# Performance work log

Measured on AMD Instinct MI355X. Metric: run time of the kernel, lower is better.

## Reference

```python
import jax, jax.numpy as jnp
import numpy as np

RNN_DIMS = 1024
FC_DIMS = 1024
N_CLASSES = 256
BATCH = 128


def setup_inputs() -> dict:
    key = jax.random.key(0)
    ks = jax.random.split(key, 10)
    s = 1.0 / np.sqrt(RNN_DIMS)
    inp = {
        "x": jax.random.normal(ks[0], (BATCH, RNN_DIMS), dtype=jnp.float32),
        "h1": jax.random.normal(ks[1], (BATCH, RNN_DIMS), dtype=jnp.float32),
        # GRUCell params (PyTorch layout: [3*H, H] stacked as r,z,n)
        "w_ih": jax.random.uniform(ks[2], (3 * RNN_DIMS, RNN_DIMS), jnp.float32, -s, s),
        "w_hh": jax.random.uniform(ks[3], (3 * RNN_DIMS, RNN_DIMS), jnp.float32, -s, s),
        "b_ih": jax.random.uniform(ks[4], (3 * RNN_DIMS,), jnp.float32, -s, s),
        "b_hh": jax.random.uniform(ks[5], (3 * RNN_DIMS,), jnp.float32, -s, s),
        "w_fc1": jax.random.uniform(ks[6], (FC_DIMS, RNN_DIMS), jnp.float32, -s, s),
        "b_fc1": jax.random.uniform(ks[7], (FC_DIMS,), jnp.float32, -s, s),
        "w_fc3": jax.random.uniform(ks[8], (N_CLASSES, FC_DIMS), jnp.float32, -1.0 / np.sqrt(FC_DIMS), 1.0 / np.sqrt(FC_DIMS)),
        "b_fc3": jax.random.uniform(ks[9], (N_CLASSES,), jnp.float32, -1.0 / np.sqrt(FC_DIMS), 1.0 / np.sqrt(FC_DIMS)),
    }
    return inp


def reference(x, h1, w_ih, w_hh, b_ih, b_hh, w_fc1, b_fc1, w_fc3, b_fc3):
    # --- GRUCell (PyTorch semantics) ---
    gi = x @ w_ih.T + b_ih          # [B, 3H]
    gh = h1 @ w_hh.T + b_hh         # [B, 3H]
    i_r, i_z, i_n = jnp.split(gi, 3, axis=-1)
    h_r, h_z, h_n = jnp.split(gh, 3, axis=-1)
    r = jax.nn.sigmoid(i_r + h_r)
    z = jax.nn.sigmoid(i_z + h_z)
    n = jnp.tanh(i_n + r * h_n)
    h1_prime = (1.0 - z) * n + z * h1   # [B, H]
    # --- residual + MLP head ---
    res = h1_prime + x
    relu1 = jax.nn.relu(res @ w_fc1.T + b_fc1)   # [B, FC]
    out = relu1 @ w_fc3.T + b_fc3                # [B, N_CLASSES]
    return (out, h1_prime)
```

## Files before the change

kernel.cpp:

```cpp
#include <hip/hip_runtime.h>
#include <math.h>

typedef short bf16x8 __attribute__((ext_vector_type(8)));
typedef float f32x4 __attribute__((ext_vector_type(4)));

__device__ __forceinline__ int cvt2(float lo, float hi) {
    int r;
    asm("v_cvt_pk_bf16_f32 %0, %1, %2" : "=v"(r) : "v"(lo), "v"(hi));
    return r;
}

#define BAR() do {                                                        \
        asm volatile("s_waitcnt lgkmcnt(0)" ::: "memory");                \
        __builtin_amdgcn_s_barrier();                                     \
        __builtin_amdgcn_sched_barrier(0);                                \
    } while (0)

__global__ __launch_bounds__(256, 2) void gates_k(
    const float* __restrict__ x, const float* __restrict__ h1,
    const float* __restrict__ w_ih, const float* __restrict__ w_hh,
    const float* __restrict__ b_ih, const float* __restrict__ b_hh,
    float* __restrict__ h1p, float* __restrict__ res,
    float* __restrict__ zf1p, float* __restrict__ zout)
{
    __shared__ short As[2][128 * 64];
    __shared__ short Ws[2][96 * 64];
    const int tid  = threadIdx.x;
    const int lane = tid & 63;
    const int wv   = tid >> 6;

    {
        int id = blockIdx.x * 256 + tid;
        f32x4 z = {};
        *(f32x4*)(zf1p + id * 4) = z;
        zout[id] = 0.0f;
    }

    const int b    = blockIdx.x;
    const int tile = (b & 7) * 8 + ((b >> 3) >> 1);
    const int rg   = (b >> 3) & 1;
    const int c0   = tile * 16;
    const int row0 = rg * 64;

    const int r0 = tid >> 3, kc = tid & 7;

    const float* aP[4];
    int saI[4];
    #pragma unroll
    for (int i = 0; i < 4; ++i) {
        int ma = r0 + 32 * i;
        const float* src = (i < 2) ? x : h1;
        aP[i] = src + (row0 + (ma & 63)) * 1024 + kc * 8;
        saI[i] = (ma * 64 + kc * 8) ^ ((ma & 7) << 3);
    }
    const float* wP[3];
    int swI[3];
    #pragma unroll
    for (int i = 0; i < 3; ++i) {
        int mw = r0 + 32 * i;
        int g = mw >> 4;
        const float* src = (g < 3) ? w_ih : w_hh;
        wP[i] = src + ((g % 3) * 1024 + c0 + (mw & 15)) * 1024 + kc * 8;
        swI[i] = (mw * 64 + kc * 8) ^ ((mw & 7) << 3);
    }

    f32x4 A[2][4][2], W[2][3][2];
    f32x4 acc[6] = {};

#define G_ISSUE(kt, s) do {                                               \
        _Pragma("unroll")                                                 \
        for (int i = 0; i < 4; ++i) {                                     \
            A[s][i][0] = *(const f32x4*)(aP[i] + (kt) * 64);              \
            A[s][i][1] = *(const f32x4*)(aP[i] + (kt) * 64 + 4);          \
        }                                                                 \
        _Pragma("unroll")                                                 \
        for (int i = 0; i < 3; ++i) {                                     \
            W[s][i][0] = *(const f32x4*)(wP[i] + (kt) * 64);              \
            W[s][i][1] = *(const f32x4*)(wP[i] + (kt) * 64 + 4);          \
        }                                                                 \
    } while (0)

#define G_STAGE(s, bb) do {                                               \
        _Pragma("unroll")                                                 \
        for (int i = 0; i < 4; ++i) {                                     \
            int4 p;                                                       \
            p.x = cvt2(A[s][i][0][0], A[s][i][0][1]);                     \
            p.y = cvt2(A[s][i][0][2], A[s][i][0][3]);                     \
            p.z = cvt2(A[s][i][1][0], A[s][i][1][1]);                     \
            p.w = cvt2(A[s][i][1][2], A[s][i][1][3]);                     \
            *(int4*)&As[bb][saI[i]] = p;                                  \
        }                                                                 \
        _Pragma("unroll")                                                 \
        for (int i = 0; i < 3; ++i) {                                     \
            int4 q;                                                       \
            q.x = cvt2(W[s][i][0][0], W[s][i][0][1]);                     \
            q.y = cvt2(W[s][i][0][2], W[s][i][0][3]);                     \
            q.z = cvt2(W[s][i][1][0], W[s][i][1][1]);                     \
            q.w = cvt2(W[s][i][1][2], W[s][i][1][3]);                     \
            *(int4*)&Ws[bb][swI[i]] = q;                                  \
        }                                                                 \
    } while (0)

#define G_COMPUTE(bb) do {                                                \
        _Pragma("unroll")                                                 \
        for (int kk = 0; kk < 64; kk += 32) {                             \
            const int kw = kk + 8 * (lane >> 4);                          \
            const int ar = wv * 16 + (lane & 15);                         \
            bf16x8 afx = *(const bf16x8*)&As[bb][(ar * 64 + kw) ^ ((ar & 7) << 3)]; \
            bf16x8 afh = *(const bf16x8*)&As[bb][((ar + 64) * 64 + kw) ^ ((ar & 7) << 3)]; \
            _Pragma("unroll")                                             \
            for (int g = 0; g < 6; ++g) {                                 \
                int br = g * 16 + (lane & 15);                            \
                bf16x8 bw = *(const bf16x8*)&Ws[bb][(br * 64 + kw) ^ ((br & 7) << 3)]; \
                acc[g] = __builtin_amdgcn_mfma_f32_16x16x32_bf16(         \
                    (g < 3) ? afx : afh, bw, acc[g], 0, 0, 0);            \
            }                                                             \
        }                                                                 \
    } while (0)

    G_ISSUE(0, 0); G_ISSUE(1, 1);

    #pragma unroll 1
    for (int kt2 = 0; kt2 < 8; ++kt2) {
        const int kt = 2 * kt2;
        G_STAGE(0, 0); if (kt + 2 < 16) G_ISSUE(kt + 2, 0); BAR(); G_COMPUTE(0);
        G_STAGE(1, 1); if (kt + 3 < 16) G_ISSUE(kt + 3, 1); BAR(); G_COMPUTE(1);
    }

#undef G_ISSUE
#undef G_STAGE
#undef G_COMPUTE

    const int j = c0 + (lane & 15);
    const float bir = b_ih[j], biz = b_ih[1024 + j], bin = b_ih[2048 + j];
    const float bhr = b_hh[j], bhz = b_hh[1024 + j], bhn = b_hh[2048 + j];
    const int rbase = row0 + wv * 16 + (lane >> 4) * 4;
    #pragma unroll
    for (int r = 0; r < 4; ++r) {
        const int row = rbase + r;
        float ir  = acc[0][r] + bir, iz = acc[1][r] + biz, inn = acc[2][r] + bin;
        float hr  = acc[3][r] + bhr, hz = acc[4][r] + bhz, hn  = acc[5][r] + bhn;
        float rr = 1.0f / (1.0f + __expf(-(ir + hr)));
        float zz = 1.0f / (1.0f + __expf(-(iz + hz)));
        float nn = tanhf(inn + rr * hn);
        float h1v = h1[row * 1024 + j];
        float hp  = (1.0f - zz) * nn + zz * h1v;
        h1p[row * 1024 + j] = hp;
        res[row * 1024 + j] = hp + x[row * 1024 + j];
    }
}

template<int NT, bool ATOMIC, bool RELUA>
__global__ __launch_bounds__(256, 2) void gemm_k(
    const float* __restrict__ act, const float* __restrict__ wgt,
    const float* __restrict__ bias,
    float* __restrict__ out, int ldo, int nkt, int ksbits)
{
    constexpr int CT = NT / 16;
    __shared__ short As[2][64 * 64];
    __shared__ short Ws[2][NT * 64];

    const int tid  = threadIdx.x;
    const int lane = tid & 63;
    const int wv   = tid >> 6;

    const int ks   = blockIdx.x & ((1 << ksbits) - 1);
    const int rest = blockIdx.x >> ksbits;
    const int rg   = rest & 1;
    const int tile = rest >> 1;
    const int c0   = tile * NT;
    const int row0 = rg * 64;
    const int kt0  = ks * nkt;

    const int r0 = tid >> 3, kc = tid & 7;
    const float* aP = act + (row0 + r0) * 1024 + kt0 * 64 + kc * 8;
    const float* wP = wgt + (c0 + r0) * 1024 + kt0 * 64 + kc * 8;
    const bool wAct = (tid < NT * 8);

    const int saI0 = (r0 * 64 + kc * 8) ^ ((r0 & 7) << 3);
    const int saI1 = ((r0 + 32) * 64 + kc * 8) ^ ((r0 & 7) << 3);

    f32x4 A[4][4], W[4][2];
    f32x4 acc[CT] = {};

#define ISSUE(kt, s) do {                                                 \
        A[s][0] = *(const f32x4*)(aP + (kt) * 64);                        \
        A[s][1] = *(const f32x4*)(aP + (kt) * 64 + 4);                    \
        A[s][2] = *(const f32x4*)(aP + (kt) * 64 + 32768);                \
        A[s][3] = *(const f32x4*)(aP + (kt) * 64 + 32772);                \
        if (wAct) {                                                       \
            W[s][0] = *(const f32x4*)(wP + (kt) * 64);                    \
            W[s][1] = *(const f32x4*)(wP + (kt) * 64 + 4);                \
        }                                                                 \
    } while (0)

#define RL(v) (RELUA ? fmaxf((v), 0.0f) : (v))

#define STAGE(s, b) do {                                                  \
        int4 p0, p1;                                                      \
        p0.x = cvt2(RL(A[s][0][0]), RL(A[s][0][1]));                      \
        p0.y = cvt2(RL(A[s][0][2]), RL(A[s][0][3]));                      \
        p0.z = cvt2(RL(A[s][1][0]), RL(A[s][1][1]));                      \
        p0.w = cvt2(RL(A[s][1][2]), RL(A[s][1][3]));                      \
        p1.x = cvt2(RL(A[s][2][0]), RL(A[s][2][1]));                      \
        p1.y = cvt2(RL(A[s][2][2]), RL(A[s][2][3]));                      \
        p1.z = cvt2(RL(A[s][3][0]), RL(A[s][3][1]));                      \
        p1.w = cvt2(RL(A[s][3][2]), RL(A[s][3][3]));                      \
        *(int4*)&As[b][saI0] = p0;                                        \
        *(int4*)&As[b][saI1] = p1;                                        \
        if (wAct) {                                                       \
            int4 q;                                                       \
            q.x = cvt2(W[s][0][0], W[s][0][1]);                           \
            q.y = cvt2(W[s][0][2], W[s][0][3]);                           \
            q.z = cvt2(W[s][1][0], W[s][1][1]);                           \
            q.w = cvt2(W[s][1][2], W[s][1][3]);                           \
            *(int4*)&Ws[b][saI0] = q;                                     \
        }                                                                 \
    } while (0)

#define COMPUTE(b) do {                                                   \
        _Pragma("unroll")                                                 \
        for (int kk = 0; kk < 64; kk += 32) {                             \
            const int kw = kk + 8 * (lane >> 4);                          \
            const int ar = wv * 16 + (lane & 15);                         \
            bf16x8 af = *(const bf16x8*)&As[b][(ar * 64 + kw) ^ ((ar & 7) << 3)]; \
            bf16x8 bw[CT];                                                \
            _Pragma("unroll")                                             \
            for (int ct = 0; ct < CT; ++ct) {                             \
                int br = ct * 16 + (lane & 15);                           \
                bw[ct] = *(const bf16x8*)&Ws[b][(br * 64 + kw) ^ ((br & 7) << 3)]; \
            }                                                             \
            _Pragma("unroll")                                             \
            for (int ct = 0; ct < CT; ++ct)                               \
                acc[ct] = __builtin_amdgcn_mfma_f32_16x16x32_bf16(        \
                    af, bw[ct], acc[ct], 0, 0, 0);                        \
        }                                                                 \
    } while (0)

    ISSUE(0, 0); ISSUE(1, 1); ISSUE(2, 2); ISSUE(3, 3);

    #pragma unroll 1
    for (int g = 0; g < nkt / 4; ++g) {
        const int kt = 4 * g;
        STAGE(0, 0); if (kt + 4 < nkt) ISSUE(kt + 4, 0); BAR(); COMPUTE(0);
        STAGE(1, 1); if (kt + 5 < nkt) ISSUE(kt + 5, 1); BAR(); COMPUTE(1);
        STAGE(2, 0); if (kt + 6 < nkt) ISSUE(kt + 6, 2); BAR(); COMPUTE(0);
        STAGE(3, 1); if (kt + 7 < nkt) ISSUE(kt + 7, 3); BAR(); COMPUTE(1);
    }

#undef ISSUE
#undef RL
#undef STAGE
#undef COMPUTE

    #pragma unroll
    for (int ct = 0; ct < CT; ++ct) {
        int col = c0 + ct * 16 + (lane & 15);
        float bv = (bias && ks == 0) ? bias[col] : 0.0f;
        #pragma unroll
        for (int r = 0; r < 4; ++r) {
            int row = row0 + wv * 16 + (lane >> 4) * 4 + r;
            float v = acc[ct][r] + bv;
            if (ATOMIC) unsafeAtomicAdd(&out[row * ldo + col], v);
            else        out[row * ldo + col] = v;
        }
    }
}

extern "C" void kernel_launch(void* const* d_in, const int* in_sizes, int n_in,
                              void* d_out, int out_size, void* d_ws, size_t ws_size,
                              hipStream_t stream)
{
    const float* x     = (const float*)d_in[0];
    const float* h1    = (const float*)d_in[1];
    const float* w_ih  = (const float*)d_in[2];
    const float* w_hh  = (const float*)d_in[3];
    const float* b_ih  = (const float*)d_in[4];
    const float* b_hh  = (const float*)d_in[5];
    const float* w_fc1 = (const float*)d_in[6];
    const float* b_fc1 = (const float*)d_in[7];
    const float* w_fc3 = (const float*)d_in[8];
    const float* b_fc3 = (const float*)d_in[9];

    float* out = (float*)d_out;
    float* h1p = out + 128 * 256;

    float* ws  = (float*)d_ws;
    float* res = ws;
    float* f1p = ws + 128 * 1024;

    gates_k<<<128, 256, 0, stream>>>(x, h1, w_ih, w_hh, b_ih, b_hh,
                                     h1p, res, f1p, out);
    gemm_k<16, true, false><<<256, 256, 0, stream>>>(
        res, w_fc1, b_fc1, f1p, 1024, 8, 1);
    gemm_k<16, true, true><<<64, 256, 0, stream>>>(
        f1p, w_fc3, b_fc3, out, 256, 8, 1);
}
```

Baseline: 30.20 us.

## Prefetch FC weights into L2 from extra blocks and deepen gate weight pipeline

Launches 128 extra blocks in the gates kernel that zero the split-K output buffers and read all of w_fc1 and w_fc3 with a dummy reduction, so the later GEMM kernels find those weights warm in L2/LLC. Gate weight loads are now issued four k-tiles ahead instead of two, using a 4-deep register buffer, while activation loads stay two ahead. The block-to-tile mapping is simplified and launch bounds drop to 1 block per CU to allow the extra registers. The cost is a lower occupancy limit and extra memory traffic competing with the gate GEMM.

```diff
diff --git a/kernel.cpp b/kernel.cpp
--- a/kernel.cpp
+++ b/kernel.cpp
@@ -16,10 +16,11 @@
         __builtin_amdgcn_sched_barrier(0);                                \
     } while (0)
 
-__global__ __launch_bounds__(256, 2) void gates_k(
+__global__ __launch_bounds__(256, 1) void gates_k(
     const float* __restrict__ x, const float* __restrict__ h1,
     const float* __restrict__ w_ih, const float* __restrict__ w_hh,
     const float* __restrict__ b_ih, const float* __restrict__ b_hh,
+    const float* __restrict__ w_fc1, const float* __restrict__ w_fc3,
     float* __restrict__ h1p, float* __restrict__ res,
     float* __restrict__ zf1p, float* __restrict__ zout)
 {
@@ -28,20 +29,32 @@
     const int tid  = threadIdx.x;
     const int lane = tid & 63;
     const int wv   = tid >> 6;
-
-    {
-        int id = blockIdx.x * 256 + tid;
+    const int b    = blockIdx.x;
+
+    if (b >= 128) {
+        const int w = b - 128;
         f32x4 z = {};
-        *(f32x4*)(zf1p + id * 4) = z;
-        zout[id] = 0.0f;
-    }
-
-    const int b    = blockIdx.x;
-    const int tile = (b & 7) * 8 + ((b >> 3) >> 1);
-    const int rg   = (b >> 3) & 1;
+        *(f32x4*)(zf1p + w * 1024 + tid * 4) = z;
+        if (tid < 64) *(f32x4*)(zout + w * 256 + tid * 4) = z;
+        float s = 0.0f;
+        const float* q = w_fc1 + (w >> 1) * 16384 + (w & 1) * 512
+                         + (tid >> 4) * 1024 + (tid & 15) * 32;
+        #pragma unroll
+        for (int i = 0; i < 8; ++i) {
+            f32x4 v = *(const f32x4*)(q + 4 * i);
+            s += v[0] + v[1] + v[2] + v[3];
+        }
+        const float* q3 = w_fc3 + w * 2048 + tid * 8;
+        f32x4 v0 = *(const f32x4*)q3, v1 = *(const f32x4*)(q3 + 4);
+        s += v0[0] + v0[1] + v0[2] + v0[3] + v1[0] + v1[1] + v1[2] + v1[3];
+        asm volatile("" :: "v"(s));
+        return;
+    }
+
+    const int tile = b & 63;
+    const int rg   = b >> 6;
     const int c0   = tile * 16;
     const int row0 = rg * 64;
-
     const int r0 = tid >> 3, kc = tid & 7;
 
     const float* aP[4];
@@ -64,15 +77,19 @@
         swI[i] = (mw * 64 + kc * 8) ^ ((mw & 7) << 3);
     }
 
-    f32x4 A[2][4][2], W[2][3][2];
+    f32x4 A[2][4][2];
+    f32x4 W[4][3][2];
     f32x4 acc[6] = {};
 
-#define G_ISSUE(kt, s) do {                                               \
+#define G_ISSUE_A(kt, s) do {                                             \
         _Pragma("unroll")                                                 \
         for (int i = 0; i < 4; ++i) {                                     \
             A[s][i][0] = *(const f32x4*)(aP[i] + (kt) * 64);              \
             A[s][i][1] = *(const f32x4*)(aP[i] + (kt) * 64 + 4);          \
         }                                                                 \
+    } while (0)
+
+#define G_ISSUE_W(kt, s) do {                                             \
         _Pragma("unroll")                                                 \
         for (int i = 0; i < 3; ++i) {                                     \
             W[s][i][0] = *(const f32x4*)(wP[i] + (kt) * 64);              \
@@ -80,23 +97,23 @@
         }                                                                 \
     } while (0)
 
-#define G_STAGE(s, bb) do {                                               \
+#define G_STAGE(sa, sw, bb) do {                                          \
         _Pragma("unroll")                                                 \
         for (int i = 0; i < 4; ++i) {                                     \
             int4 p;                                                       \
-            p.x = cvt2(A[s][i][0][0], A[s][i][0][1]);                     \
-            p.y = cvt2(A[s][i][0][2], A[s][i][0][3]);                     \
-            p.z = cvt2(A[s][i][1][0], A[s][i][1][1]);                     \
-            p.w = cvt2(A[s][i][1][2], A[s][i][1][3]);                     \
+            p.x = cvt2(A[sa][i][0][0], A[sa][i][0][1]);                   \
+            p.y = cvt2(A[sa][i][0][2], A[sa][i][0][3]);                   \
+            p.z = cvt2(A[sa][i][1][0], A[sa][i][1][1]);                   \
+            p.w = cvt2(A[sa][i][1][2], A[sa][i][1][3]);                   \
             *(int4*)&As[bb][saI[i]] = p;                                  \
         }                                                                 \
         _Pragma("unroll")                                                 \
         for (int i = 0; i < 3; ++i) {                                     \
             int4 q;                                                       \
-            q.x = cvt2(W[s][i][0][0], W[s][i][0][1]);                     \
-            q.y = cvt2(W[s][i][0][2], W[s][i][0][3]);                     \
-            q.z = cvt2(W[s][i][1][0], W[s][i][1][1]);                     \
-            q.w = cvt2(W[s][i][1][2], W[s][i][1][3]);                     \
+            q.x = cvt2(W[sw][i][0][0], W[sw][i][0][1]);                   \
+            q.y = cvt2(W[sw][i][0][2], W[sw][i][0][3]);                   \
+            q.z = cvt2(W[sw][i][1][0], W[sw][i][1][1]);                   \
+            q.w = cvt2(W[sw][i][1][2], W[sw][i][1][3]);                   \
             *(int4*)&Ws[bb][swI[i]] = q;                                  \
         }                                                                 \
     } while (0)
@@ -118,18 +135,30 @@
         }                                                                 \
     } while (0)
 
-    G_ISSUE(0, 0); G_ISSUE(1, 1);
+#define G_STEP(k, sw, sa, bb) do {                                        \
+        G_STAGE(sa, sw, bb);                                              \
+        if ((k) + 4 < 16) G_ISSUE_W((k) + 4, sw);                         \
+        if ((k) + 2 < 16) G_ISSUE_A((k) + 2, sa);                         \
+        BAR();                                                            \
+        G_COMPUTE(bb);                                                    \
+    } while (0)
+
+    G_ISSUE_W(0, 0); G_ISSUE_W(1, 1); G_ISSUE_W(2, 2); G_ISSUE_W(3, 3);
+    G_ISSUE_A(0, 0); G_ISSUE_A(1, 1);
 
     #pragma unroll 1
-    for (int kt2 = 0; kt2 < 8; ++kt2) {
-        const int kt = 2 * kt2;
-        G_STAGE(0, 0); if (kt + 2 < 16) G_ISSUE(kt + 2, 0); BAR(); G_COMPUTE(0);
-        G_STAGE(1, 1); if (kt + 3 < 16) G_ISSUE(kt + 3, 1); BAR(); G_COMPUTE(1);
-    }
-
-#undef G_ISSUE
+    for (int kt0 = 0; kt0 < 16; kt0 += 4) {
+        G_STEP(kt0 + 0, 0, 0, 0);
+        G_STEP(kt0 + 1, 1, 1, 1);
+        G_STEP(kt0 + 2, 2, 0, 0);
+        G_STEP(kt0 + 3, 3, 1, 1);
+    }
+
+#undef G_ISSUE_A
+#undef G_ISSUE_W
 #undef G_STAGE
 #undef G_COMPUTE
+#undef G_STEP
 
     const int j = c0 + (lane & 15);
     const float bir = b_ih[j], biz = b_ih[1024 + j], bin = b_ih[2048 + j];
@@ -289,8 +318,8 @@
     float* res = ws;
     float* f1p = ws + 128 * 1024;
 
-    gates_k<<<128, 256, 0, stream>>>(x, h1, w_ih, w_hh, b_ih, b_hh,
-                                     h1p, res, f1p, out);
+    gates_k<<<256, 256, 0, stream>>>(x, h1, w_ih, w_hh, b_ih, b_hh,
+                                     w_fc1, w_fc3, h1p, res, f1p, out);
     gemm_k<16, true, false><<<256, 256, 0, stream>>>(
         res, w_fc1, b_fc1, f1p, 1024, 8, 1);
     gemm_k<16, true, true><<<64, 256, 0, stream>>>(
```

Result: slower. 32.99 us (+9.2%).

## Pre-convert FC weights and residual to bf16 in extra gates-kernel blocks

Applied to the files above, without the earlier changes.

Adds 128 extra blocks to the gates kernel that zero the accumulation buffers and convert w_fc1 and w_fc3 from fp32 to bf16 in workspace. The GRU epilogue now writes the residual as bf16. The FC GEMMs then load bf16 weights and activations directly instead of converting fp32 in registers. This halves global load bytes and removes conversion ALU work in the GEMMs. The cost is that every call must still read the fp32 weights and write bf16 copies, and the first kernel gains more blocks.

```diff
diff --git a/kernel.cpp b/kernel.cpp
--- a/kernel.cpp
+++ b/kernel.cpp
@@ -20,28 +20,52 @@
     const float* __restrict__ x, const float* __restrict__ h1,
     const float* __restrict__ w_ih, const float* __restrict__ w_hh,
     const float* __restrict__ b_ih, const float* __restrict__ b_hh,
-    float* __restrict__ h1p, float* __restrict__ res,
-    float* __restrict__ zf1p, float* __restrict__ zout)
+    const float* __restrict__ w_fc1, const float* __restrict__ w_fc3,
+    float* __restrict__ h1p, short* __restrict__ resb,
+    float* __restrict__ f1p, float* __restrict__ outz,
+    short* __restrict__ w1b, short* __restrict__ w3b)
 {
     __shared__ short As[2][128 * 64];
     __shared__ short Ws[2][96 * 64];
     const int tid  = threadIdx.x;
     const int lane = tid & 63;
     const int wv   = tid >> 6;
-
-    {
-        int id = blockIdx.x * 256 + tid;
+    const int b    = blockIdx.x;
+
+    if (b >= 128) {
+        const int w = b - 128;
         f32x4 z = {};
-        *(f32x4*)(zf1p + id * 4) = z;
-        zout[id] = 0.0f;
-    }
-
-    const int b    = blockIdx.x;
-    const int tile = (b & 7) * 8 + ((b >> 3) >> 1);
-    const int rg   = (b >> 3) & 1;
+        *(f32x4*)(f1p + w * 1024 + tid * 4) = z;
+        if (tid < 64) *(f32x4*)(outz + w * 256 + tid * 4) = z;
+        {
+            const float* s = w_fc1 + w * 8192 + tid * 32;
+            short*       d = w1b   + w * 8192 + tid * 32;
+            #pragma unroll
+            for (int i = 0; i < 4; ++i) {
+                f32x4 v0 = *(const f32x4*)(s + i * 8);
+                f32x4 v1 = *(const f32x4*)(s + i * 8 + 4);
+                int4 p;
+                p.x = cvt2(v0[0], v0[1]); p.y = cvt2(v0[2], v0[3]);
+                p.z = cvt2(v1[0], v1[1]); p.w = cvt2(v1[2], v1[3]);
+                *(int4*)(d + i * 8) = p;
+            }
+        }
+        {
+            const float* s = w_fc3 + w * 2048 + tid * 8;
+            short*       d = w3b   + w * 2048 + tid * 8;
+            f32x4 v0 = *(const f32x4*)s, v1 = *(const f32x4*)(s + 4);
+            int4 p;
+            p.x = cvt2(v0[0], v0[1]); p.y = cvt2(v0[2], v0[3]);
+            p.z = cvt2(v1[0], v1[1]); p.w = cvt2(v1[2], v1[3]);
+            *(int4*)d = p;
+        }
+        return;
+    }
+
+    const int tile = b & 63;
+    const int rg   = b >> 6;
     const int c0   = tile * 16;
     const int row0 = rg * 64;
-
     const int r0 = tid >> 3, kc = tid & 7;
 
     const float* aP[4];
@@ -119,14 +143,12 @@
     } while (0)
 
     G_ISSUE(0, 0); G_ISSUE(1, 1);
-
     #pragma unroll 1
     for (int kt2 = 0; kt2 < 8; ++kt2) {
         const int kt = 2 * kt2;
         G_STAGE(0, 0); if (kt + 2 < 16) G_ISSUE(kt + 2, 0); BAR(); G_COMPUTE(0);
         G_STAGE(1, 1); if (kt + 3 < 16) G_ISSUE(kt + 3, 1); BAR(); G_COMPUTE(1);
     }
-
 #undef G_ISSUE
 #undef G_STAGE
 #undef G_COMPUTE
@@ -146,13 +168,14 @@
         float h1v = h1[row * 1024 + j];
         float hp  = (1.0f - zz) * nn + zz * h1v;
         h1p[row * 1024 + j] = hp;
-        res[row * 1024 + j] = hp + x[row * 1024 + j];
+        float rv = hp + x[row * 1024 + j];
+        resb[row * 1024 + j] = (short)cvt2(rv, rv);
     }
 }
 
-template<int NT, bool ATOMIC, bool RELUA>
+template<int NT, bool ABF16, bool RELUA>
 __global__ __launch_bounds__(256, 2) void gemm_k(
-    const float* __restrict__ act, const float* __restrict__ wgt,
+    const void* __restrict__ actv, const short* __restrict__ wgt,
     const float* __restrict__ bias,
     float* __restrict__ out, int ldo, int nkt, int ksbits)
 {
@@ -173,49 +196,52 @@
     const int kt0  = ks * nkt;
 
     const int r0 = tid >> 3, kc = tid & 7;
-    const float* aP = act + (row0 + r0) * 1024 + kt0 * 64 + kc * 8;
-    const float* wP = wgt + (c0 + r0) * 1024 + kt0 * 64 + kc * 8;
+    const float* aPf = (const float*)actv + (row0 + r0) * 1024 + kt0 * 64 + kc * 8;
+    const short* aPb = (const short*)actv + (row0 + r0) * 1024 + kt0 * 64 + kc * 8;
+    const short* wP  = wgt + (c0 + r0) * 1024 + kt0 * 64 + kc * 8;
     const bool wAct = (tid < NT * 8);
 
-    const int saI0 = (r0 * 64 + kc * 8) ^ ((r0 & 7) << 3);
-    const int saI1 = ((r0 + 32) * 64 + kc * 8) ^ ((r0 & 7) << 3);
-
-    f32x4 A[4][4], W[4][2];
+    const int sa0 = (r0 * 64 + kc * 8) ^ ((r0 & 7) << 3);
+    const int sa1 = ((r0 + 32) * 64 + kc * 8) ^ ((r0 & 7) << 3);
+
+    f32x4 Af[4][4];
+    int4  Ab[4][2];
+    int4  Wb[4];
     f32x4 acc[CT] = {};
 
 #define ISSUE(kt, s) do {                                                 \
-        A[s][0] = *(const f32x4*)(aP + (kt) * 64);                        \
-        A[s][1] = *(const f32x4*)(aP + (kt) * 64 + 4);                    \
-        A[s][2] = *(const f32x4*)(aP + (kt) * 64 + 32768);                \
-        A[s][3] = *(const f32x4*)(aP + (kt) * 64 + 32772);                \
-        if (wAct) {                                                       \
-            W[s][0] = *(const f32x4*)(wP + (kt) * 64);                    \
-            W[s][1] = *(const f32x4*)(wP + (kt) * 64 + 4);                \
-        }                                                                 \
+        if constexpr (ABF16) {                                            \
+            Ab[s][0] = *(const int4*)(aPb + (kt) * 64);                   \
+            Ab[s][1] = *(const int4*)(aPb + (kt) * 64 + 32 * 1024);       \
+        } else {                                                          \
+            Af[s][0] = *(const f32x4*)(aPf + (kt) * 64);                  \
+            Af[s][1] = *(const f32x4*)(aPf + (kt) * 64 + 4);              \
+            Af[s][2] = *(const f32x4*)(aPf + (kt) * 64 + 32768);          \
+            Af[s][3] = *(const f32x4*)(aPf + (kt) * 64 + 32772);          \
+        }                                                                 \
+        if (wAct) Wb[s] = *(const int4*)(wP + (kt) * 64);                 \
     } while (0)
 
 #define RL(v) (RELUA ? fmaxf((v), 0.0f) : (v))
 
 #define STAGE(s, b) do {                                                  \
-        int4 p0, p1;                                                      \
-        p0.x = cvt2(RL(A[s][0][0]), RL(A[s][0][1]));                      \
-        p0.y = cvt2(RL(A[s][0][2]), RL(A[s][0][3]));                      \
-        p0.z = cvt2(RL(A[s][1][0]), RL(A[s][1][1]));                      \
-        p0.w = cvt2(RL(A[s][1][2]), RL(A[s][1][3]));                      \
-        p1.x = cvt2(RL(A[s][2][0]), RL(A[s][2][1]));                      \
-        p1.y = cvt2(RL(A[s][2][2]), RL(A[s][2][3]));                      \
-        p1.z = cvt2(RL(A[s][3][0]), RL(A[s][3][1]));                      \
-        p1.w = cvt2(RL(A[s][3][2]), RL(A[s][3][3]));                      \
-        *(int4*)&As[b][saI0] = p0;                                        \
-        *(int4*)&As[b][saI1] = p1;                                        \
-        if (wAct) {                                                       \
-            int4 q;                                                       \
-            q.x = cvt2(W[s][0][0], W[s][0][1]);                           \
-            q.y = cvt2(W[s][0][2], W[s][0][3]);                           \
-            q.z = cvt2(W[s][1][0], W[s][1][1]);                           \
-            q.w = cvt2(W[s][1][2], W[s][1][3]);                           \
-            *(int4*)&Ws[b][saI0] = q;                                     \
-        }                                                                 \
+        if constexpr (ABF16) {                                            \
+            *(int4*)&As[b][sa0] = Ab[s][0];                               \
+            *(int4*)&As[b][sa1] = Ab[s][1];                               \
+        } else {                                                          \
+            int4 p0, p1;                                                  \
+            p0.x = cvt2(RL(Af[s][0][0]), RL(Af[s][0][1]));                \
+            p0.y = cvt2(RL(Af[s][0][2]), RL(Af[s][0][3]));                \
+            p0.z = cvt2(RL(Af[s][1][0]), RL(Af[s][1][1]));                \
+            p0.w = cvt2(RL(Af[s][1][2]), RL(Af[s][1][3]));                \
+            p1.x = cvt2(RL(Af[s][2][0]), RL(Af[s][2][1]));                \
+            p1.y = cvt2(RL(Af[s][2][2]), RL(Af[s][2][3]));                \
+            p1.z = cvt2(RL(Af[s][3][0]), RL(Af[s][3][1]));                \
+            p1.w = cvt2(RL(Af[s][3][2]), RL(Af[s][3][3]));                \
+            *(int4*)&As[b][sa0] = p0;                                     \
+            *(int4*)&As[b][sa1] = p1;                                     \
+        }                                                                 \
+        if (wAct) *(int4*)&Ws[b][sa0] = Wb[s];                            \
     } while (0)
 
 #define COMPUTE(b) do {                                                   \
@@ -260,9 +286,7 @@
         #pragma unroll
         for (int r = 0; r < 4; ++r) {
             int row = row0 + wv * 16 + (lane >> 4) * 4 + r;
-            float v = acc[ct][r] + bv;
-            if (ATOMIC) unsafeAtomicAdd(&out[row * ldo + col], v);
-            else        out[row * ldo + col] = v;
+            unsafeAtomicAdd(&out[row * ldo + col], acc[ct][r] + bv);
         }
     }
 }
@@ -285,14 +309,17 @@
     float* out = (float*)d_out;
     float* h1p = out + 128 * 256;
 
-    float* ws  = (float*)d_ws;
-    float* res = ws;
-    float* f1p = ws + 128 * 1024;
-
-    gates_k<<<128, 256, 0, stream>>>(x, h1, w_ih, w_hh, b_ih, b_hh,
-                                     h1p, res, f1p, out);
+    char* ws = (char*)d_ws;
+    short* resb = (short*)ws;
+    float* f1p  = (float*)(ws + 256 * 1024);
+    short* w1b  = (short*)(ws + 768 * 1024);
+    short* w3b  = (short*)(ws + 768 * 1024 + 2 * 1024 * 1024);
+
+    gates_k<<<256, 256, 0, stream>>>(x, h1, w_ih, w_hh, b_ih, b_hh,
+                                     w_fc1, w_fc3, h1p, resb, f1p, out,
+                                     w1b, w3b);
     gemm_k<16, true, false><<<256, 256, 0, stream>>>(
-        res, w_fc1, b_fc1, f1p, 1024, 8, 1);
-    gemm_k<16, true, true><<<64, 256, 0, stream>>>(
-        f1p, w_fc3, b_fc3, out, 256, 8, 1);
+        resb, w1b, b_fc1, f1p, 1024, 8, 1);
+    gemm_k<16, false, true><<<64, 256, 0, stream>>>(
+        f1p, w3b, b_fc3, out, 256, 8, 1);
 }
```

Measured after the change: 42.39 us. +40.3%, slower.

## Fuse GRU gates and both FC GEMMs into one persistent kernel with grid barriers

Applied to the files above, without the earlier changes.

Replaces the three kernel launches with one 256-block kernel (plus a tiny barrier-init kernel). Gates run on 128 blocks while the other 128 zero the accumulation buffers, then software grid barriers separate the fc1 and fc3 phases. The aim is to remove launch gaps and inter-kernel drain between dependent stages. In exchange it adds atomic-spin barriers that require all 256 blocks to be co-resident, and the gates phase runs at occupancy 1 with half the grid idle.

```diff
diff --git a/kernel.cpp b/kernel.cpp
--- a/kernel.cpp
+++ b/kernel.cpp
@@ -16,56 +16,169 @@
         __builtin_amdgcn_sched_barrier(0);                                \
     } while (0)
 
-__global__ __launch_bounds__(256, 2) void gates_k(
+__device__ __forceinline__ void gsync(int* cnt, int* gen) {
+    __syncthreads();
+    if (threadIdx.x == 0) {
+        __builtin_amdgcn_fence(__ATOMIC_RELEASE, "agent");
+        int g0 = __hip_atomic_load(gen, __ATOMIC_RELAXED, __HIP_MEMORY_SCOPE_AGENT);
+        int v  = __hip_atomic_fetch_add(cnt, 1, __ATOMIC_RELAXED, __HIP_MEMORY_SCOPE_AGENT);
+        if (v == 255) {
+            __hip_atomic_fetch_add(gen, 1, __ATOMIC_RELAXED, __HIP_MEMORY_SCOPE_AGENT);
+        } else {
+            while (__hip_atomic_load(gen, __ATOMIC_RELAXED, __HIP_MEMORY_SCOPE_AGENT) == g0)
+                __builtin_amdgcn_s_sleep(4);
+        }
+    }
+    __syncthreads();
+    __builtin_amdgcn_fence(__ATOMIC_ACQUIRE, "agent");
+}
+
+__global__ void init_k(int* bar) {
+    if (threadIdx.x < 4) bar[threadIdx.x] = 0;
+}
+
+template<bool RELUA>
+__device__ __forceinline__ void fc_phase(
+    const float* __restrict__ act, const float* __restrict__ wgt,
+    const float* __restrict__ bias, float* __restrict__ outp, int ldo,
+    int bb, int tid, short* As0, short* As1, short* Ws0, short* Ws1)
+{
+    const int lane = tid & 63;
+    const int wv   = tid >> 6;
+    const int ks = bb & 1, rest = bb >> 1, rg = rest & 1, tile = rest >> 1;
+    const int c0 = tile * 16, row0 = rg * 64, kt0 = ks * 8;
+    const int r0 = tid >> 3, kc = tid & 7;
+    const float* aP = act + (row0 + r0) * 1024 + kt0 * 64 + kc * 8;
+    const float* wP = wgt + (c0 + r0) * 1024 + kt0 * 64 + kc * 8;
+    const bool wAct = (tid < 128);
+    const int sa0 = (r0 * 64 + kc * 8) ^ ((r0 & 7) << 3);
+    const int sa1 = ((r0 + 32) * 64 + kc * 8) ^ ((r0 & 7) << 3);
+
+    f32x4 A[4][4], W[4][2];
+    f32x4 acc = {};
+
+#define F_ISSUE(kt, s) do {                                               \
+        A[s][0] = *(const f32x4*)(aP + (kt) * 64);                        \
+        A[s][1] = *(const f32x4*)(aP + (kt) * 64 + 4);                    \
+        A[s][2] = *(const f32x4*)(aP + (kt) * 64 + 32768);                \
+        A[s][3] = *(const f32x4*)(aP + (kt) * 64 + 32772);                \
+        if (wAct) {                                                       \
+            W[s][0] = *(const f32x4*)(wP + (kt) * 64);                    \
+            W[s][1] = *(const f32x4*)(wP + (kt) * 64 + 4);                \
+        }                                                                 \
+    } while (0)
+
+#define RL(v) (RELUA ? fmaxf((v), 0.0f) : (v))
+
+#define F_STAGE(s, AS, WS) do {                                           \
+        int4 p0, p1;                                                      \
+        p0.x = cvt2(RL(A[s][0][0]), RL(A[s][0][1]));                      \
+        p0.y = cvt2(RL(A[s][0][2]), RL(A[s][0][3]));                      \
+        p0.z = cvt2(RL(A[s][1][0]), RL(A[s][1][1]));                      \
+        p0.w = cvt2(RL(A[s][1][2]), RL(A[s][1][3]));                      \
+        p1.x = cvt2(RL(A[s][2][0]), RL(A[s][2][1]));                      \
+        p1.y = cvt2(RL(A[s][2][2]), RL(A[s][2][3]));                      \
+        p1.z = cvt2(RL(A[s][3][0]), RL(A[s][3][1]));                      \
+        p1.w = cvt2(RL(A[s][3][2]), RL(A[s][3][3]));                      \
+        *(int4*)&AS[sa0] = p0;                                            \
+        *(int4*)&AS[sa1] = p1;                                            \
+        if (wAct) {                                                       \
+            int4 q;                                                       \
+            q.x = cvt2(W[s][0][0], W[s][0][1]);                           \
+            q.y = cvt2(W[s][0][2], W[s][0][3]);                           \
+            q.z = cvt2(W[s][1][0], W[s][1][1]);                           \
+            q.w = cvt2(W[s][1][2], W[s][1][3]);                           \
+            *(int4*)&WS[sa0] = q;                                         \
+        }                                                                 \
+    } while (0)
+
+#define F_COMPUTE(AS, WS) do {                                            \
+        _Pragma("unroll")                                                 \
+        for (int kk = 0; kk < 64; kk += 32) {                             \
+            const int kw = kk + 8 * (lane >> 4);                          \
+            const int ar = wv * 16 + (lane & 15);                         \
+            bf16x8 af = *(const bf16x8*)&AS[(ar * 64 + kw) ^ ((ar & 7) << 3)]; \
+            int br = lane & 15;                                           \
+            bf16x8 bw = *(const bf16x8*)&WS[(br * 64 + kw) ^ ((br & 7) << 3)]; \
+            acc = __builtin_amdgcn_mfma_f32_16x16x32_bf16(af, bw, acc, 0, 0, 0); \
+        }                                                                 \
+    } while (0)
+
+    F_ISSUE(0, 0); F_ISSUE(1, 1); F_ISSUE(2, 2); F_ISSUE(3, 3);
+
+    #pragma unroll 1
+    for (int g = 0; g < 2; ++g) {
+        const int kt = 4 * g;
+        F_STAGE(0, As0, Ws0); if (kt + 4 < 8) F_ISSUE(kt + 4, 0); BAR(); F_COMPUTE(As0, Ws0);
+        F_STAGE(1, As1, Ws1); if (kt + 5 < 8) F_ISSUE(kt + 5, 1); BAR(); F_COMPUTE(As1, Ws1);
+        F_STAGE(2, As0, Ws0); if (kt + 6 < 8) F_ISSUE(kt + 6, 2); BAR(); F_COMPUTE(As0, Ws0);
+        F_STAGE(3, As1, Ws1); if (kt + 7 < 8) F_ISSUE(kt + 7, 3); BAR(); F_COMPUTE(As1, Ws1);
+    }
+
+#undef F_ISSUE
+#undef RL
+#undef F_STAGE
+#undef F_COMPUTE
+
+    const int col = c0 + (lane & 15);
+    const float bv = (ks == 0) ? bias[col] : 0.0f;
+    #pragma unroll
+    for (int r = 0; r < 4; ++r) {
+        int row = row0 + wv * 16 + (lane >> 4) * 4 + r;
+        unsafeAtomicAdd(&outp[row * ldo + col], acc[r] + bv);
+    }
+}
+
+__global__ __launch_bounds__(256, 1) void fused_k(
     const float* __restrict__ x, const float* __restrict__ h1,
     const float* __restrict__ w_ih, const float* __restrict__ w_hh,
     const float* __restrict__ b_ih, const float* __restrict__ b_hh,
-    float* __restrict__ h1p, float* __restrict__ res,
-    float* __restrict__ zf1p, float* __restrict__ zout)
+    const float* __restrict__ w_fc1, const float* __restrict__ b_fc1,
+    const float* __restrict__ w_fc3, const float* __restrict__ b_fc3,
+    float* __restrict__ out, float* __restrict__ h1p,
+    float* __restrict__ res, float* __restrict__ f1p, int* bar)
 {
     __shared__ short As[2][128 * 64];
     __shared__ short Ws[2][96 * 64];
     const int tid  = threadIdx.x;
     const int lane = tid & 63;
     const int wv   = tid >> 6;
-
-    {
-        int id = blockIdx.x * 256 + tid;
+    const int b    = blockIdx.x;
+
+    if (b >= 128) {
+        const int w = b - 128;
         f32x4 z = {};
-        *(f32x4*)(zf1p + id * 4) = z;
-        zout[id] = 0.0f;
-    }
-
-    const int b    = blockIdx.x;
-    const int tile = (b & 7) * 8 + ((b >> 3) >> 1);
-    const int rg   = (b >> 3) & 1;
-    const int c0   = tile * 16;
-    const int row0 = rg * 64;
-
-    const int r0 = tid >> 3, kc = tid & 7;
-
-    const float* aP[4];
-    int saI[4];
-    #pragma unroll
-    for (int i = 0; i < 4; ++i) {
-        int ma = r0 + 32 * i;
-        const float* src = (i < 2) ? x : h1;
-        aP[i] = src + (row0 + (ma & 63)) * 1024 + kc * 8;
-        saI[i] = (ma * 64 + kc * 8) ^ ((ma & 7) << 3);
-    }
-    const float* wP[3];
-    int swI[3];
-    #pragma unroll
-    for (int i = 0; i < 3; ++i) {
-        int mw = r0 + 32 * i;
-        int g = mw >> 4;
-        const float* src = (g < 3) ? w_ih : w_hh;
-        wP[i] = src + ((g % 3) * 1024 + c0 + (mw & 15)) * 1024 + kc * 8;
-        swI[i] = (mw * 64 + kc * 8) ^ ((mw & 7) << 3);
-    }
-
-    f32x4 A[2][4][2], W[2][3][2];
-    f32x4 acc[6] = {};
+        *(f32x4*)(f1p + w * 1024 + tid * 4) = z;
+        if (tid < 64) *(f32x4*)(out + w * 256 + tid * 4) = z;
+    } else {
+        const int tile = b & 63;
+        const int rg   = b >> 6;
+        const int c0   = tile * 16;
+        const int row0 = rg * 64;
+        const int r0 = tid >> 3, kc = tid & 7;
+
+        const float* aP[4];
+        int saI[4];
+        #pragma unroll
+        for (int i = 0; i < 4; ++i) {
+            int ma = r0 + 32 * i;
+            const float* src = (i < 2) ? x : h1;
+            aP[i] = src + (row0 + (ma & 63)) * 1024 + kc * 8;
+            saI[i] = (ma * 64 + kc * 8) ^ ((ma & 7) << 3);
+        }
+        const float* wP[3];
+        int swI[3];
+        #pragma unroll
+        for (int i = 0; i < 3; ++i) {
+            int mw = r0 + 32 * i;
+            int g = mw >> 4;
+            const float* src = (g < 3) ? w_ih : w_hh;
+            wP[i] = src + ((g % 3) * 1024 + c0 + (mw & 15)) * 1024 + kc * 8;
+            swI[i] = (mw * 64 + kc * 8) ^ ((mw & 7) << 3);
+        }
+
+        f32x4 A[2][4][2], W[2][3][2];
+        f32x4 acc[6] = {};
 
 #define G_ISSUE(kt, s) do {                                               \
         _Pragma("unroll")                                                 \
@@ -118,152 +231,46 @@
         }                                                                 \
     } while (0)
 
-    G_ISSUE(0, 0); G_ISSUE(1, 1);
-
-    #pragma unroll 1
-    for (int kt2 = 0; kt2 < 8; ++kt2) {
-        const int kt = 2 * kt2;
-        G_STAGE(0, 0); if (kt + 2 < 16) G_ISSUE(kt + 2, 0); BAR(); G_COMPUTE(0);
-        G_STAGE(1, 1); if (kt + 3 < 16) G_ISSUE(kt + 3, 1); BAR(); G_COMPUTE(1);
-    }
-
+        G_ISSUE(0, 0); G_ISSUE(1, 1);
+        #pragma unroll 1
+        for (int kt2 = 0; kt2 < 8; ++kt2) {
+            const int kt = 2 * kt2;
+            G_STAGE(0, 0); if (kt + 2 < 16) G_ISSUE(kt + 2, 0); BAR(); G_COMPUTE(0);
+            G_STAGE(1, 1); if (kt + 3 < 16) G_ISSUE(kt + 3, 1); BAR(); G_COMPUTE(1);
+        }
 #undef G_ISSUE
 #undef G_STAGE
 #undef G_COMPUTE
 
-    const int j = c0 + (lane & 15);
-    const float bir = b_ih[j], biz = b_ih[1024 + j], bin = b_ih[2048 + j];
-    const float bhr = b_hh[j], bhz = b_hh[1024 + j], bhn = b_hh[2048 + j];
-    const int rbase = row0 + wv * 16 + (lane >> 4) * 4;
-    #pragma unroll
-    for (int r = 0; r < 4; ++r) {
-        const int row = rbase + r;
-        float ir  = acc[0][r] + bir, iz = acc[1][r] + biz, inn = acc[2][r] + bin;
-        float hr  = acc[3][r] + bhr, hz = acc[4][r] + bhz, hn  = acc[5][r] + bhn;
-        float rr = 1.0f / (1.0f + __expf(-(ir + hr)));
-        float zz = 1.0f / (1.0f + __expf(-(iz + hz)));
-        float nn = tanhf(inn + rr * hn);
-        float h1v = h1[row * 1024 + j];
-        float hp  = (1.0f - zz) * nn + zz * h1v;
-        h1p[row * 1024 + j] = hp;
-        res[row * 1024 + j] = hp + x[row * 1024 + j];
-    }
-}
-
-template<int NT, bool ATOMIC, bool RELUA>
-__global__ __launch_bounds__(256, 2) void gemm_k(
-    const float* __restrict__ act, const float* __restrict__ wgt,
-    const float* __restrict__ bias,
-    float* __restrict__ out, int ldo, int nkt, int ksbits)
-{
-    constexpr int CT = NT / 16;
-    __shared__ short As[2][64 * 64];
-    __shared__ short Ws[2][NT * 64];
-
-    const int tid  = threadIdx.x;
-    const int lane = tid & 63;
-    const int wv   = tid >> 6;
-
-    const int ks   = blockIdx.x & ((1 << ksbits) - 1);
-    const int rest = blockIdx.x >> ksbits;
-    const int rg   = rest & 1;
-    const int tile = rest >> 1;
-    const int c0   = tile * NT;
-    const int row0 = rg * 64;
-    const int kt0  = ks * nkt;
-
-    const int r0 = tid >> 3, kc = tid & 7;
-    const float* aP = act + (row0 + r0) * 1024 + kt0 * 64 + kc * 8;
-    const float* wP = wgt + (c0 + r0) * 1024 + kt0 * 64 + kc * 8;
-    const bool wAct = (tid < NT * 8);
-
-    const int saI0 = (r0 * 64 + kc * 8) ^ ((r0 & 7) << 3);
-    const int saI1 = ((r0 + 32) * 64 + kc * 8) ^ ((r0 & 7) << 3);
-
-    f32x4 A[4][4], W[4][2];
-    f32x4 acc[CT] = {};
-
-#define ISSUE(kt, s) do {                                                 \
-        A[s][0] = *(const f32x4*)(aP + (kt) * 64);                        \
-        A[s][1] = *(const f32x4*)(aP + (kt) * 64 + 4);                    \
-        A[s][2] = *(const f32x4*)(aP + (kt) * 64 + 32768);                \
-        A[s][3] = *(const f32x4*)(aP + (kt) * 64 + 32772);                \
-        if (wAct) {                                                       \
-            W[s][0] = *(const f32x4*)(wP + (kt) * 64);                    \
-            W[s][1] = *(const f32x4*)(wP + (kt) * 64 + 4);                \
-        }                                                                 \
-    } while (0)
-
-#define RL(v) (RELUA ? fmaxf((v), 0.0f) : (v))
-
-#define STAGE(s, b) do {                                                  \
-        int4 p0, p1;                                                      \
-        p0.x = cvt2(RL(A[s][0][0]), RL(A[s][0][1]));                      \
-        p0.y = cvt2(RL(A[s][0][2]), RL(A[s][0][3]));                      \
-        p0.z = cvt2(RL(A[s][1][0]), RL(A[s][1][1]));                      \
-        p0.w = cvt2(RL(A[s][1][2]), RL(A[s][1][3]));                      \
-        p1.x = cvt2(RL(A[s][2][0]), RL(A[s][2][1]));                      \
-        p1.y = cvt2(RL(A[s][2][2]), RL(A[s][2][3]));                      \
-        p1.z = cvt2(RL(A[s][3][0]), RL(A[s][3][1]));                      \
-        p1.w = cvt2(RL(A[s][3][2]), RL(A[s][3][3]));                      \
-        *(int4*)&As[b][saI0] = p0;                                        \
-        *(int4*)&As[b][saI1] = p1;                                        \
-        if (wAct) {                                                       \
-            int4 q;                                                       \
-            q.x = cvt2(W[s][0][0], W[s][0][1]);                           \
-            q.y = cvt2(W[s][0][2], W[s][0][3]);                           \
-            q.z = cvt2(W[s][1][0], W[s][1][1]);                           \
-            q.w = cvt2(W[s][1][2], W[s][1][3]);                           \
-            *(int4*)&Ws[b][saI0] = q;                                     \
-        }                                                                 \
-    } while (0)
-
-#define COMPUTE(b) do {                                                   \
-        _Pragma("unroll")                                                 \
-        for (int kk = 0; kk < 64; kk += 32) {                             \
-            const int kw = kk + 8 * (lane >> 4);                          \
-            const int ar = wv * 16 + (lane & 15);                         \
-            bf16x8 af = *(const bf16x8*)&As[b][(ar * 64 + kw) ^ ((ar & 7) << 3)]; \
-            bf16x8 bw[CT];                                                \
-            _Pragma("unroll")                                             \
-            for (int ct = 0; ct < CT; ++ct) {                             \
-                int br = ct * 16 + (lane & 15);                           \
-                bw[ct] = *(const bf16x8*)&Ws[b][(br * 64 + kw) ^ ((br & 7) << 3)]; \
-            }                                                             \
-            _Pragma("unroll")                                             \
-            for (int ct = 0; ct < CT; ++ct)                               \
-                acc[ct] = __builtin_amdgcn_mfma_f32_16x16x32_bf16(        \
-                    af, bw[ct], acc[ct], 0, 0, 0);                        \
-        }                                                                 \
-    } while (0)
-
-    ISSUE(0, 0); ISSUE(1, 1); ISSUE(2, 2); ISSUE(3, 3);
-
-    #pragma unroll 1
-    for (int g = 0; g < nkt / 4; ++g) {
-        const int kt = 4 * g;
-        STAGE(0, 0); if (kt + 4 < nkt) ISSUE(kt + 4, 0); BAR(); COMPUTE(0);
-        STAGE(1, 1); if (kt + 5 < nkt) ISSUE(kt + 5, 1); BAR(); COMPUTE(1);
-        STAGE(2, 0); if (kt + 6 < nkt) ISSUE(kt + 6, 2); BAR(); COMPUTE(0);
-        STAGE(3, 1); if (kt + 7 < nkt) ISSUE(kt + 7, 3); BAR(); COMPUTE(1);
-    }
-
-#undef ISSUE
-#undef RL
-#undef STAGE
-#undef COMPUTE
-
-    #pragma unroll
-    for (int ct = 0; ct < CT; ++ct) {
-        int col = c0 + ct * 16 + (lane & 15);
-        float bv = (bias && ks == 0) ? bias[col] : 0.0f;
+        const int j = c0 + (lane & 15);
+        const float bir = b_ih[j], biz = b_ih[1024 + j], bin = b_ih[2048 + j];
+        const float bhr = b_hh[j], bhz = b_hh[1024 + j], bhn = b_hh[2048 + j];
+        const int rbase = row0 + wv * 16 + (lane >> 4) * 4;
         #pragma unroll
         for (int r = 0; r < 4; ++r) {
-            int row = row0 + wv * 16 + (lane >> 4) * 4 + r;
-            float v = acc[ct][r] + bv;
-            if (ATOMIC) unsafeAtomicAdd(&out[row * ldo + col], v);
-            else        out[row * ldo + col] = v;
-        }
+            const int row = rbase + r;
+            float ir  = acc[0][r] + bir, iz = acc[1][r] + biz, inn = acc[2][r] + bin;
+            float hr  = acc[3][r] + bhr, hz = acc[4][r] + bhz, hn  = acc[5][r] + bhn;
+            float rr = 1.0f / (1.0f + __expf(-(ir + hr)));
+            float zz = 1.0f / (1.0f + __expf(-(iz + hz)));
+            float nn = tanhf(inn + rr * hn);
+            float h1v = h1[row * 1024 + j];
+            float hp  = (1.0f - zz) * nn + zz * h1v;
+            h1p[row * 1024 + j] = hp;
+            res[row * 1024 + j] = hp + x[row * 1024 + j];
+        }
+    }
+
+    gsync(bar, bar + 1);
+
+    fc_phase<false>(res, w_fc1, b_fc1, f1p, 1024, b, tid,
+                    As[0], As[1], Ws[0], Ws[1]);
+
+    gsync(bar + 2, bar + 3);
+
+    if (b < 64) {
+        fc_phase<true>(f1p, w_fc3, b_fc3, out, 256, b, tid,
+                       As[0], As[1], Ws[0], Ws[1]);
     }
 }
 
@@ -287,12 +294,11 @@
 
     float* ws  = (float*)d_ws;
     float* res = ws;
-    float* f1p = ws + 128 * 1024;
-
-    gates_k<<<128, 256, 0, stream>>>(x, h1, w_ih, w_hh, b_ih, b_hh,
-                                     h1p, res, f1p, out);
-    gemm_k<16, true, false><<<256, 256, 0, stream>>>(
-        res, w_fc1, b_fc1, f1p, 1024, 8, 1);
-    gemm_k<16, true, true><<<64, 256, 0, stream>>>(
-        f1p, w_fc3, b_fc3, out, 256, 8, 1);
-}
+    float* f1p = ws + 131072;
+    int*   bar = (int*)(ws + 262144);
+
+    init_k<<<1, 64, 0, stream>>>(bar);
+    fused_k<<<256, 256, 0, stream>>>(x, h1, w_ih, w_hh, b_ih, b_hh,
+                                     w_fc1, b_fc1, w_fc3, b_fc3,
+                                     out, h1p, res, f1p, bar);
+}
```

Result: slower. 71.68 us (+137.3%).
